# Optimization experiments

Measured on AMD Instinct MI355X. Metric: run time of the kernel, lower is better.

The kernel has to match this reference:

```python
import jax, jax.numpy as jnp
import numpy as np

B, N, K, NUM_CLASSES = 8, 4096, 20, 40


def _knn_idx(x, k):
    # x: [B, N, D] -> indices of k nearest neighbors (self excluded), [B, N, k]
    sq = jnp.sum(x * x, axis=-1)  # [B, N]
    dist = sq[:, :, None] + sq[:, None, :] - 2.0 * jnp.einsum('bnd,bmd->bnm', x, x)
    dist = jnp.where(jnp.eye(x.shape[1], dtype=bool)[None], jnp.inf, dist)
    return jax.lax.top_k(-dist, k)[1]


def _edge_conv(x, idx, params):
    # PyG EdgeConv with max aggregation: max_j MLP([x_i, x_j - x_i])
    x_j = jax.vmap(lambda xb, ib: xb[ib])(x, idx)              # [B, N, K, D]
    x_i = jnp.broadcast_to(x[:, :, None, :], x_j.shape)        # [B, N, K, D]
    h = jnp.concatenate([x_i, x_j - x_i], axis=-1)             # [B, N, K, 2D]
    for w, b in params:
        h = jax.nn.relu(h @ w + b)
    return jnp.max(h, axis=2)                                  # [B, N, out]


def setup_inputs() -> dict:
    key = jax.random.key(0)
    ks = jax.random.split(key, 12)

    def lin(k, i, o):  # torch Linear default init
        k1, k2 = jax.random.split(k)
        s = 1.0 / np.sqrt(i)
        return (jax.random.uniform(k1, (i, o), jnp.float32, -s, s),
                jax.random.uniform(k2, (o,), jnp.float32, -s, s))

    inp = {
        'pos': jax.random.normal(ks[0], (B * N, 3), jnp.float32),
        'batch': jnp.repeat(jnp.arange(B, dtype=jnp.int32), N),
    }
    names = [('m1w1', 'm1b1', 6, 64), ('m1w2', 'm1b2', 64, 64), ('m1w3', 'm1b3', 64, 64),
             ('m2w1', 'm2b1', 128, 128), ('m2w2', 'm2b2', 128, 128), ('m2w3', 'm2b3', 128, 256),
             ('lin0_w', 'lin0_b', 256, 512), ('lin1_w', 'lin1_b', 512, 256),
             ('lin2_w', 'lin2_b', 256, 256), ('lin3_w', 'lin3_b', 256, NUM_CLASSES)]
    for t, (wn, bn, i, o) in enumerate(names):
        w, b = lin(ks[t + 1], i, o)
        inp[wn] = w
        inp[bn] = b
    return inp


def reference(pos, batch, m1w1, m1b1, m1w2, m1b2, m1w3, m1b3,
              m2w1, m2b1, m2w2, m2b2, m2w3, m2b3,
              lin0_w, lin0_b, lin1_w, lin1_b, lin2_w, lin2_b, lin3_w, lin3_b):
    x = pos.reshape(B, N, 3)
    x = _edge_conv(x, _knn_idx(x, K), [(m1w1, m1b1), (m1w2, m1b2), (m1w3, m1b3)])   # [B,N,64]
    x = _edge_conv(x, _knn_idx(x, K), [(m2w1, m2b1), (m2w2, m2b2), (m2w3, m2b3)])   # [B,N,256]
    x = jax.nn.relu(x @ lin0_w + lin0_b)                                            # [B,N,512]
    x = jax.ops.segment_max(x.reshape(B * N, -1), batch, num_segments=B)            # [B,512]
    x = jax.nn.relu(x @ lin1_w + lin1_b)
    x = jax.nn.relu(x @ lin2_w + lin2_b)   # dropout is identity in eval mode
    x = x @ lin3_w + lin3_b
    return jax.nn.log_softmax(x, axis=-1)
```

## Files before the change

kernel.cpp:

```cpp
#include <hip/hip_runtime.h>

#define DEVI static __device__ __forceinline__

typedef __attribute__((ext_vector_type(4))) float f32x4;
typedef __attribute__((ext_vector_type(8))) short short8;
typedef __attribute__((ext_vector_type(4))) short short4v;
typedef __attribute__((ext_vector_type(4))) unsigned uint4v;
typedef __attribute__((ext_vector_type(8))) __bf16 bf16x8;

#define N_    4096
#define KNN_  20
#define NPTS  32768

DEVI unsigned short f2bf(float f){
  unsigned u = __float_as_uint(f);
  u += 0x7FFFu + ((u >> 16) & 1u);
  return (unsigned short)(u >> 16);
}
DEVI float bf2f(unsigned short s){ return __uint_as_float(((unsigned)s) << 16); }
DEVI float bf2fs(short s){ return __uint_as_float(((unsigned)(unsigned short)s) << 16); }
DEVI unsigned umin32(unsigned a, unsigned b){ return a < b ? a : b; }
DEVI unsigned umax32(unsigned a, unsigned b){ return a > b ? a : b; }

DEVI f32x4 mfma16(short8 a, short8 b, f32x4 c){
  return __builtin_amdgcn_mfma_f32_16x16x32_bf16(
      __builtin_bit_cast(bf16x8, a), __builtin_bit_cast(bf16x8, b), c, 0, 0, 0);
}

DEVI short8 lds_frag(const unsigned short* buf, int row, int k0, int strideS, int swzMask){
  return *(const short8*)(buf + row*strideS + (k0 ^ ((row & swzMask) << 3)));
}
DEVI void lds_put8(unsigned short* buf, int row, int k0, int strideS, int swzMask, short8 v){
  *(short8*)(buf + row*strideS + (k0 ^ ((row & swzMask) << 3))) = v;
}
DEVI void lds_put1(unsigned short* buf, int row, int col, int strideS, int swzMask, unsigned short v){
  buf[row*strideS + (col ^ ((row & swzMask) << 3))] = v;
}

DEVI void ins32(unsigned K, unsigned (&a)[20]){
#pragma unroll
  for (int t = 19; t >= 1; --t) a[t] = umin32(a[t], umax32(a[t-1], K));
  a[0] = umin32(a[0], K);
}
DEVI void ins64(double K, double (&a)[20]){
#pragma unroll
  for (int t = 19; t >= 1; --t) a[t] = fmin(a[t], fmax(a[t-1], K));
  a[0] = fmin(a[0], K);
}

__global__ __launch_bounds__(256) void p3_k(const float* __restrict__ pos,
    unsigned short* __restrict__ p3h, unsigned short* __restrict__ p3l, float* __restrict__ nrm3){
  int p = blockIdx.x*256 + threadIdx.x;
  if (p >= NPTS) return;
  float x = pos[(size_t)p*3], y = pos[(size_t)p*3+1], z = pos[(size_t)p*3+2];
  float v[8] = {x, y, z, 0.f, 0.f, 0.f, 0.f, 0.f};
#pragma unroll
  for (int c = 0; c < 8; ++c){
    unsigned short h = f2bf(v[c]);
    p3h[(size_t)p*8 + c] = h;
    p3l[(size_t)p*8 + c] = f2bf(v[c] - bf2f(h));
  }
  nrm3[p] = fmaf(x, x, fmaf(y, y, z*z));
}

template<int MODE>
__global__ __launch_bounds__(256) void knn_k(const unsigned short* __restrict__ Xh,
                                             const unsigned short* __restrict__ Xl,
                                             const float* __restrict__ nrm,
                                             unsigned* __restrict__ pk){
  constexpr int OBL  = MODE ? 8192  : 1024;
  constexpr int OS   = MODE ? 16384 : 2048;
  constexpr int OBUF = OS + 17408;
  constexpr int OTHR = OBUF + 6144;
  constexpr int OSQ  = OTHR + 256;
  __shared__ __align__(16) char smem[OSQ + 256];
  unsigned short* Bh = (unsigned short*)(smem);
  unsigned short* Bl = (unsigned short*)(smem + OBL);
  unsigned* S        = (unsigned*)(smem + OS);
  unsigned* buf      = (unsigned*)(smem + OBUF);
  unsigned* rowThr   = (unsigned*)(smem + OTHR);
  float* sqj         = (float*)(smem + OSQ);
  unsigned* mD       = (unsigned*)(smem);

  const int blk = blockIdx.x;
  const int rt = blk & 63, ch = (blk >> 6) & 1, bb = blk >> 7;
  const int rowbase = rt * 64, cbase = ch * 2048;
  const size_t gb = (size_t)bb * N_;
  const int tid = threadIdx.x, lane = tid & 63, wid = tid >> 6;
  const int l15 = lane & 15, kL = (lane >> 4) << 3, r0 = (lane >> 4) << 2;

  if (tid < 64) rowThr[tid] = 0xFFFFFFFFu;

  short8 ah0 = {0,0,0,0,0,0,0,0}, ah1 = {0,0,0,0,0,0,0,0};
  short8 al0 = {0,0,0,0,0,0,0,0}, al1 = {0,0,0,0,0,0,0,0};
  const int arow = rowbase + (wid << 4) + l15;
  if (MODE == 1){
    const size_t ab = (gb + arow) * 64;
    ah0 = *(const short8*)(Xh + ab + kL);
    ah1 = *(const short8*)(Xh + ab + 32 + kL);
    al0 = *(const short8*)(Xl + ab + kL);
    al1 = *(const short8*)(Xl + ab + 32 + kL);
  } else {
    if (lane < 16){
      const size_t ab = (gb + arow) * 8;
      ah0 = *(const short8*)(Xh + ab);
      al0 = *(const short8*)(Xl + ab);
    }
  }
  float sqi[4];
#pragma unroll
  for (int r = 0; r < 4; ++r) sqi[r] = nrm[gb + rowbase + (wid << 4) + r0 + r];

  unsigned arr[20];
#pragma unroll
  for (int t = 0; t < 20; ++t) arr[t] = 0xFFFFFFFFu;
  int cnt = 0;
  const int srow = tid & 63, q = tid >> 6;

  if (MODE == 1){
    for (int f = tid; f < 512; f += 256){
      int lf = f & 63, half = (f >> 6) & 1, nt = f >> 7;
      int row = nt*16 + (lf & 15);
      int col = half*32 + ((lf >> 4) << 3);
      const size_t src = (gb + cbase + row) * 64 + col;
      *(short8*)(Bh + f*8) = *(const short8*)(Xh + src);
      *(short8*)(Bl + f*8) = *(const short8*)(Xl + src);
    }
  } else {
    if (tid < 64)       *(short8*)(Bh + tid*8)      = *(const short8*)(Xh + (gb + cbase + tid)*8);
    else if (tid < 128) *(short8*)(Bl + (tid-64)*8) = *(const short8*)(Xl + (gb + cbase + (tid-64))*8);
  }
  if (tid < 64) sqj[tid] = nrm[gb + cbase + tid];
  __syncthreads();

  for (int c = 0; c < 32; ++c){
    const bool selfTile = (cbase + c*64 == rowbase);
#pragma unroll
    for (int nt = 0; nt < 4; ++nt){
      f32x4 acc = {0.f,0.f,0.f,0.f};
      if (MODE == 1){
        const int fb = lane*8;
        short8 bh0 = *(const short8*)(Bh + (nt*2+0)*512 + fb);
        short8 bh1 = *(const short8*)(Bh + (nt*2+1)*512 + fb);
        short8 bl0 = *(const short8*)(Bl + (nt*2+0)*512 + fb);
        short8 bl1 = *(const short8*)(Bl + (nt*2+1)*512 + fb);
        acc = mfma16(ah0, bh0, acc); acc = mfma16(ah1, bh1, acc);
        acc = mfma16(ah0, bl0, acc); acc = mfma16(ah1, bl1, acc);
        acc = mfma16(al0, bh0, acc); acc = mfma16(al1, bh1, acc);
      } else {
        int br = nt*16 + l15;
        short8 bh = {0,0,0,0,0,0,0,0}, bl = {0,0,0,0,0,0,0,0};
        if (lane < 16){
          bh = *(const short8*)(Bh + br*8);
          bl = *(const short8*)(Bl + br*8);
        }
        acc = mfma16(ah0, bh, acc);
        acc = mfma16(ah0, bl, acc);
        acc = mfma16(al0, bh, acc);
      }
      int col = nt*16 + l15;
      float sj = sqj[col];
      unsigned cid = (unsigned)(c*64 + col);
#pragma unroll
      for (int r = 0; r < 4; ++r){
        int row = (wid << 4) + r0 + r;
        float dv = fmaxf(fmaf(-2.f, acc[r], sqi[r] + sj), 0.f);
        unsigned kb = (__float_as_uint(dv) & ~0x7FFu) | cid;
        if (selfTile && col == row) kb = 0x7F800000u | cid;
        S[row*68 + col] = kb;
      }
    }
    short8 nh0 = {0,0,0,0,0,0,0,0}, nh1 = {0,0,0,0,0,0,0,0};
    short8 nl0 = {0,0,0,0,0,0,0,0}, nl1 = {0,0,0,0,0,0,0,0};
    float nsq = 0.f;
    const bool more = (c + 1 < 32);
    if (more){
      if (MODE == 1){
#pragma unroll
        for (int ff = 0; ff < 2; ++ff){
          int f = tid + ff*256;
          int lf = f & 63, half = (f >> 6) & 1, nt = f >> 7;
          int row = nt*16 + (lf & 15);
          int col = half*32 + ((lf >> 4) << 3);
          const size_t src = (gb + cbase + (c+1)*64 + row) * 64 + col;
          if (ff == 0){ nh0 = *(const short8*)(Xh + src); nl0 = *(const short8*)(Xl + src); }
          else        { nh1 = *(const short8*)(Xh + src); nl1 = *(const short8*)(Xl + src); }
        }
      } else {
        if (tid < 64)       nh0 = *(const short8*)(Xh + (gb + cbase + (c+1)*64 + tid)*8);
        else if (tid < 128) nl0 = *(const short8*)(Xl + (gb + cbase + (c+1)*64 + (tid-64))*8);
      }
      if (tid < 64) nsq = nrm[gb + cbase + (c+1)*64 + tid];
    }
    __syncthreads();
    if (more){
      if (MODE == 1){
        *(short8*)(Bh + tid*8)       = nh0;
        *(short8*)(Bh + (tid+256)*8) = nh1;
        *(short8*)(Bl + tid*8)       = nl0;
        *(short8*)(Bl + (tid+256)*8) = nl1;
      } else {
        if (tid < 64)       *(short8*)(Bh + tid*8)      = nh0;
        else if (tid < 128) *(short8*)(Bl + (tid-64)*8) = nl0;
      }
      if (tid < 64) sqj[tid] = nsq;
    }
    {
      unsigned thrP = rowThr[srow];
      const uint4v* Sr4 = (const uint4v*)(S + srow*68 + q*16);
#pragma unroll
      for (int u4 = 0; u4 < 4; ++u4){
        uint4v v = Sr4[u4];
#pragma unroll
        for (int e = 0; e < 4; ++e){
          unsigned kb = v[e];
          if (kb < thrP){
            if (cnt < 6){ buf[cnt*256 + tid] = kb; ++cnt; }
            else ins32(kb, arr);
          }
        }
      }
      for (int t = 0; t < cnt; ++t) ins32(buf[t*256 + tid], arr);
      cnt = 0;
      atomicMin(&rowThr[srow], arr[19]);
    }
    __syncthreads();
  }
  if (q > 0){
#pragma unroll
    for (int t = 0; t < 20; ++t) mD[(srow*3 + q-1)*20 + t] = arr[t];
  }
  __syncthreads();
  if (q == 0){
    for (int qq = 0; qq < 3; ++qq)
#pragma unroll
      for (int t = 0; t < 20; ++t) ins32(mD[(srow*3 + qq)*20 + t], arr);
    const size_t gp = gb + rowbase + srow;
#pragma unroll
    for (int t = 0; t < 20; ++t) pk[((size_t)(ch*20 + t))*NPTS + gp] = arr[t];
  }
}

__global__ __launch_bounds__(256) void knn_merge_k(const unsigned* __restrict__ pk,
                                                   int* __restrict__ idx){
  const int p = blockIdx.x*256 + threadIdx.x;
  double arr[20];
#pragma unroll
  for (int t = 0; t < 20; ++t){
    unsigned k = pk[(size_t)t*NPTS + p];
    unsigned long long K = (((unsigned long long)(k & ~0x7FFu)) << 1) | (k & 0x7FFu);
    arr[t] = __builtin_bit_cast(double, K);
  }
#pragma unroll
  for (int t = 0; t < 20; ++t){
    unsigned k = pk[(size_t)(20 + t)*NPTS + p];
    unsigned long long K = (((unsigned long long)(k & ~0x7FFu)) << 1) | (2048u + (k & 0x7FFu));
    ins64(__builtin_bit_cast(double, K), arr);
  }
  int* o = idx + (size_t)p*KNN_;
#pragma unroll
  for (int t = 0; t < 20; ++t)
    o[t] = (int)(__builtin_bit_cast(unsigned long long, arr[t]) & 0xFFFu);
}

__global__ void stage_w_k(const float* __restrict__ src, unsigned short* __restrict__ dh,
                          unsigned short* __restrict__ dl, int K, int Nw, int KT, int NT){
  int tid = blockIdx.x*256 + threadIdx.x;
  if (tid >= NT*KT*64) return;
  int l = tid & 63;
  int kk = (tid >> 6) % KT;
  int nt = tid / (64*KT);
  int n = nt*16 + (l & 15);
  int kb = kk*32 + ((l >> 4) << 3);
#pragma unroll
  for (int e=0;e<8;++e){
    int k = kb + e;
    float w = (k < K) ? src[(size_t)k*Nw + n] : 0.f;
    unsigned short h = f2bf(w);
    dh[(size_t)tid*8 + e] = h;
    if (dl) dl[(size_t)tid*8 + e] = f2bf(w - bf2f(h));
  }
}

__global__ __launch_bounds__(256) void ec1_k(const float* __restrict__ pos, const int* __restrict__ idx1,
    const unsigned short* __restrict__ W1h, const unsigned short* __restrict__ W1l,
    const unsigned short* __restrict__ W2h, const unsigned short* __restrict__ W2l,
    const unsigned short* __restrict__ W3h, const unsigned short* __restrict__ W3l,
    const float* __restrict__ b1, const float* __restrict__ b2, const float* __restrict__ b3,
    unsigned short* __restrict__ x1h, unsigned short* __restrict__ x1l, float* __restrict__ nrm1){
  __shared__ __align__(16) char smem[52224];
  unsigned short* Ah  = (unsigned short*)(smem);
  unsigned short* Al  = (unsigned short*)(smem + 5120);
  unsigned short* H1h = (unsigned short*)(smem + 10240);
  unsigned short* H1l = (unsigned short*)(smem + 20480);
  unsigned short* H2h = (unsigned short*)(smem + 30720);
  unsigned short* H2l = (unsigned short*)(smem + 40960);
  unsigned* pmax = (unsigned*)(smem + 51200);
  const int p0 = blockIdx.x * 4;
  const int bb = p0 >> 12;
  const int tid = threadIdx.x, lane = tid & 63, wid = tid >> 6;
  pmax[tid] = 0u;
  if (tid < 80){
    int p = p0 + tid/20, slot = tid%20;
    int j = idx1[(size_t)p*KNN_ + slot];
    int gj = (bb << 12) + j;
    float a6[6];
    a6[0] = pos[(size_t)p*3]; a6[1] = pos[(size_t)p*3+1]; a6[2] = pos[(size_t)p*3+2];
    a6[3] = pos[(size_t)gj*3]   - a6[0];
    a6[4] = pos[(size_t)gj*3+1] - a6[1];
    a6[5] = pos[(size_t)gj*3+2] - a6[2];
#pragma unroll
    for (int q=0;q<4;++q){
      short8 vh, vl;
#pragma unroll
      for (int c=0;c<8;++c){
        int cc = q*8+c;
        float v = 0.f;
        if (cc < 6) v = a6[cc];
        unsigned short h = f2bf(v);
        vh[c] = (short)h;
        vl[c] = (short)f2bf(v - bf2f(h));
      }
      lds_put8(Ah, tid, q*8, 32, 3, vh);
      lds_put8(Al, tid, q*8, 32, 3, vl);
    }
  }
  __syncthreads();
  const int l15 = lane & 15, kL = (lane >> 4) << 3, r0 = (lane >> 4) << 2;
  {
    int nt = wid;
    short8 wh = *(const short8*)(W1h + ((size_t)nt*64 + lane)*8);
    short8 wl = *(const short8*)(W1l + ((size_t)nt*64 + lane)*8);
    float bias = b1[nt*16 + l15];
    for (int mt=0; mt<5; ++mt){
      int ar = mt*16 + l15;
      short8 ah = lds_frag(Ah, ar, kL, 32, 3);
      short8 al = lds_frag(Al, ar, kL, 32, 3);
      f32x4 acc = {0.f,0.f,0.f,0.f};
      acc = mfma16(ah, wh, acc);
      acc = mfma16(ah, wl, acc);
      acc = mfma16(al, wh, acc);
#pragma unroll
      for (int r=0;r<4;++r){
        int row = mt*16 + r0 + r;
        float v = fmaxf(acc[r] + bias, 0.f);
        unsigned short h = f2bf(v);
        lds_put1(H1h, row, nt*16+l15, 64, 7, h);
        lds_put1(H1l, row, nt*16+l15, 64, 7, f2bf(v - bf2f(h)));
      }
    }
  }
  __syncthreads();
  {
    int nt = wid;
    short8 wh0 = *(const short8*)(W2h + ((size_t)(nt*2+0)*64 + lane)*8);
    short8 wh1 = *(const short8*)(W2h + ((size_t)(nt*2+1)*64 + lane)*8);
    short8 wl0 = *(const short8*)(W2l + ((size_t)(nt*2+0)*64 + lane)*8);
    short8 wl1 = *(const short8*)(W2l + ((size_t)(nt*2+1)*64 + lane)*8);
    float bias = b2[nt*16 + l15];
    for (int mt=0; mt<5; ++mt){
      int ar = mt*16 + l15;
      short8 ah0 = lds_frag(H1h, ar, kL,      64, 7);
      short8 ah1 = lds_frag(H1h, ar, 32 + kL, 64, 7);
      short8 al0 = lds_frag(H1l, ar, kL,      64, 7);
      short8 al1 = lds_frag(H1l, ar, 32 + kL, 64, 7);
      f32x4 acc = {0.f,0.f,0.f,0.f};
      acc = mfma16(ah0, wh0, acc); acc = mfma16(ah1, wh1, acc);
      acc = mfma16(ah0, wl0, acc); acc = mfma16(ah1, wl1, acc);
      acc = mfma16(al0, wh0, acc); acc = mfma16(al1, wh1, acc);
#pragma unroll
      for (int r=0;r<4;++r){
        int row = mt*16 + r0 + r;
        float v = fmaxf(acc[r] + bias, 0.f);
        unsigned short h = f2bf(v);
        lds_put1(H2h, row, nt*16+l15, 64, 7, h);
        lds_put1(H2l, row, nt*16+l15, 64, 7, f2bf(v - bf2f(h)));
      }
    }
  }
  __syncthreads();
  {
    int nt = wid;
    short8 wh0 = *(const short8*)(W3h + ((size_t)(nt*2+0)*64 + lane)*8);
    short8 wh1 = *(const short8*)(W3h + ((size_t)(nt*2+1)*64 + lane)*8);
    short8 wl0 = *(const short8*)(W3l + ((size_t)(nt*2+0)*64 + lane)*8);
    short8 wl1 = *(const short8*)(W3l + ((size_t)(nt*2+1)*64 + lane)*8);
    float bias = b3[nt*16 + l15];
    for (int mt=0; mt<5; ++mt){
      int ar = mt*16 + l15;
      short8 ah0 = lds_frag(H2h, ar, kL,      64, 7);
      short8 ah1 = lds_frag(H2h, ar, 32 + kL, 64, 7);
      short8 al0 = lds_frag(H2l, ar, kL,      64, 7);
      short8 al1 = lds_frag(H2l, ar, 32 + kL, 64, 7);
      f32x4 acc = {0.f,0.f,0.f,0.f};
      acc = mfma16(ah0, wh0, acc); acc = mfma16(ah1, wh1, acc);
      acc = mfma16(ah0, wl0, acc); acc = mfma16(ah1, wl1, acc);
      acc = mfma16(al0, wh0, acc); acc = mfma16(al1, wh1, acc);
#pragma unroll
      for (int r=0;r<4;++r){
        int row = mt*16 + r0 + r;
        float v = fmaxf(acc[r] + bias, 0.f);
        atomicMax(&pmax[(row/20)*64 + nt*16 + l15], __float_as_uint(v));
      }
    }
  }
  __syncthreads();
  if (tid < 128){
    int p = tid >> 5, cp = tid & 31;
    int c0 = cp*2, c1 = c0 + 1;
    float m0 = __uint_as_float(pmax[p*64 + c0]);
    float m1 = __uint_as_float(pmax[p*64 + c1]);
    int gp = p0 + p;
    unsigned short h0 = f2bf(m0), h1v = f2bf(m1);
    x1h[(size_t)gp*64 + c0] = h0;
    x1h[(size_t)gp*64 + c1] = h1v;
    x1l[(size_t)gp*64 + c0] = f2bf(m0 - bf2f(h0));
    x1l[(size_t)gp*64 + c1] = f2bf(m1 - bf2f(h1v));
    float s = fmaf(m0, m0, m1*m1);
    s += __shfl_xor(s, 1, 32); s += __shfl_xor(s, 2, 32); s += __shfl_xor(s, 4, 32);
    s += __shfl_xor(s, 8, 32); s += __shfl_xor(s, 16, 32);
    if (cp == 0) nrm1[gp] = s;
  }
}

__global__ __launch_bounds__(256) void ec2_k(const unsigned short* __restrict__ x1h, const int* __restrict__ idx2,
    const unsigned short* __restrict__ V1, const unsigned short* __restrict__ V2, const unsigned short* __restrict__ V3,
    const float* __restrict__ b1, const float* __restrict__ b2, const float* __restrict__ b3,
    unsigned short* __restrict__ x2b){
  __shared__ __align__(16) char smem[81920];
  unsigned short* A  = (unsigned short*)(smem);
  unsigned short* H1 = (unsigned short*)(smem + 40960);
  const int p0 = blockIdx.x * 8, bb = p0 >> 12;
  const int tid = threadIdx.x, lane = tid & 63, wid = tid >> 6;
  const int l15 = lane & 15, r0 = (lane >> 4) << 2;

  if (tid < 160){
    int p = p0 + tid/20, slot = tid%20;
    int j = idx2[(size_t)p*KNN_ + slot];
    int gj = (bb << 12) + j;
    const unsigned short* xi = x1h + (size_t)p*64;
    const unsigned short* xj = x1h + (size_t)gj*64;
    int mt = tid >> 4, lrow = tid & 15;
#pragma unroll
    for (int q=0;q<8;++q){
      short8 vi = *(const short8*)(xi + q*8);
      short8 vj = *(const short8*)(xj + q*8);
      short8 vd;
#pragma unroll
      for (int c=0;c<8;++c) vd[c] = (short)f2bf(bf2fs(vj[c]) - bf2fs(vi[c]));
      *(short8*)(A + (((mt*4 + (q>>2))*64) + (q&3)*16 + lrow)*8) = vi;
      *(short8*)(A + (((mt*4 + 2 + (q>>2))*64) + (q&3)*16 + lrow)*8) = vd;
    }
  }
  __syncthreads();

  {
    short8 w[2][4];
#pragma unroll
    for (int ni=0;ni<2;++ni)
#pragma unroll
      for (int kk=0;kk<4;++kk)
        w[ni][kk] = *(const short8*)(V1 + ((size_t)((wid*2+ni)*4+kk)*64 + lane)*8);
    f32x4 b4[2];
    b4[0] = *(const f32x4*)(b1 + (wid*2+0)*16 + r0);
    b4[1] = *(const f32x4*)(b1 + (wid*2+1)*16 + r0);
    for (int mt=0; mt<10; ++mt){
      short8 bfr[4];
#pragma unroll
      for (int kk=0;kk<4;++kk) bfr[kk] = *(const short8*)(A + ((mt*4+kk)*64 + lane)*8);
#pragma unroll
      for (int ni=0;ni<2;++ni){
        int nt = wid*2 + ni;
        f32x4 acc = {0.f,0.f,0.f,0.f};
#pragma unroll
        for (int kk=0;kk<4;++kk) acc = mfma16(w[ni][kk], bfr[kk], acc);
        short4v v4;
#pragma unroll
        for (int r=0;r<4;++r) v4[r] = (short)f2bf(fmaxf(acc[r] + b4[ni][r], 0.f));
        int kk2 = nt >> 1, sub2 = (nt & 1)*2 + (r0 >> 3);
        *(short4v*)(H1 + ((mt*4+kk2)*64 + sub2*16 + l15)*8 + (r0 & 4)) = v4;
      }
    }
  }
  __syncthreads();
  {
    short8 w[2][4];
#pragma unroll
    for (int ni=0;ni<2;++ni)
#pragma unroll
      for (int kk=0;kk<4;++kk)
        w[ni][kk] = *(const short8*)(V2 + ((size_t)((wid*2+ni)*4+kk)*64 + lane)*8);
    f32x4 b4[2];
    b4[0] = *(const f32x4*)(b2 + (wid*2+0)*16 + r0);
    b4[1] = *(const f32x4*)(b2 + (wid*2+1)*16 + r0);
    for (int mt=0; mt<10; ++mt){
      short8 bfr[4];
#pragma unroll
      for (int kk=0;kk<4;++kk) bfr[kk] = *(const short8*)(H1 + ((mt*4+kk)*64 + lane)*8);
#pragma unroll
      for (int ni=0;ni<2;++ni){
        int nt = wid*2 + ni;
        f32x4 acc = {0.f,0.f,0.f,0.f};
#pragma unroll
        for (int kk=0;kk<4;++kk) acc = mfma16(w[ni][kk], bfr[kk], acc);
        short4v v4;
#pragma unroll
        for (int r=0;r<4;++r) v4[r] = (short)f2bf(fmaxf(acc[r] + b4[ni][r], 0.f));
        int kk2 = nt >> 1, sub2 = (nt & 1)*2 + (r0 >> 3);
        *(short4v*)(A + ((mt*4+kk2)*64 + sub2*16 + l15)*8 + (r0 & 4)) = v4;
      }
    }
  }
  __syncthreads();
  for (int g2=0; g2<2; ++g2){
    {
      short8 w[2][4];
#pragma unroll
      for (int ni=0;ni<2;++ni)
#pragma unroll
        for (int kk=0;kk<4;++kk)
          w[ni][kk] = *(const short8*)(V3 + ((size_t)((g2*8 + wid*2+ni)*4+kk)*64 + lane)*8);
      f32x4 b4[2];
      b4[0] = *(const f32x4*)(b3 + (g2*8 + wid*2+0)*16 + r0);
      b4[1] = *(const f32x4*)(b3 + (g2*8 + wid*2+1)*16 + r0);
      for (int mt=0; mt<10; ++mt){
        short8 bfr[4];
#pragma unroll
        for (int kk=0;kk<4;++kk) bfr[kk] = *(const short8*)(A + ((mt*4+kk)*64 + lane)*8);
#pragma unroll
        for (int ni=0;ni<2;++ni){
          int ntl = wid*2 + ni;
          f32x4 acc = {0.f,0.f,0.f,0.f};
#pragma unroll
          for (int kk=0;kk<4;++kk) acc = mfma16(w[ni][kk], bfr[kk], acc);
          short4v v4;
#pragma unroll
          for (int r=0;r<4;++r) v4[r] = (short)f2bf(fmaxf(acc[r] + b4[ni][r], 0.f));
          int kk2 = ntl >> 1, sub2 = (ntl & 1)*2 + (r0 >> 3);
          *(short4v*)(H1 + ((mt*4+kk2)*64 + sub2*16 + l15)*8 + (r0 & 4)) = v4;
        }
      }
    }
    __syncthreads();
    if (tid < 128){
      int p = tid >> 4, c8 = tid & 15;
      int kk = c8 >> 2, sub = c8 & 3;
      unsigned short mx[8];
#pragma unroll
      for (int e=0;e<8;++e) mx[e] = 0;
      for (int e=0;e<20;++e){
        int ee = e + p + c8; ee -= (ee >= 20) ? 20 : 0; ee -= (ee >= 20) ? 20 : 0;
        int row = p*20 + ee;
        short8 v = *(const short8*)(H1 + (((row>>4)*4 + kk)*64 + sub*16 + (row & 15))*8);
#pragma unroll
        for (int k2=0;k2<8;++k2){
          unsigned short u = (unsigned short)v[k2];
          mx[k2] = u > mx[k2] ? u : mx[k2];
        }
      }
      short8 o;
#pragma unroll
      for (int k2=0;k2<8;++k2) o[k2] = (short)mx[k2];
      *(short8*)(x2b + (size_t)(p0 + p)*256 + g2*128 + c8*8) = o;
    }
    __syncthreads();
  }
}

__global__ __launch_bounds__(256) void lin0_k(const unsigned short* __restrict__ x2b, const unsigned short* __restrict__ W0s,
                                              const float* __restrict__ b0, unsigned* __restrict__ pool){
  __shared__ __align__(16) char smem[67584];
  unsigned short* A = (unsigned short*)(smem);
  unsigned* ploc = (unsigned*)(smem + 65536);
  const int blk = blockIdx.x; const size_t row0 = (size_t)blk * 128; const int bb = blk >> 5;
  const int tid = threadIdx.x, lane = tid & 63, wid = tid >> 6;
  for (int it = tid; it < 4096; it += 256){
    int row = it >> 5, q = (it & 31) << 3;
    lds_put8(A, row, q, 256, 7, *(const short8*)(x2b + (row0 + row)*256 + q));
  }
  ploc[tid] = 0u; ploc[tid+256] = 0u;
  __syncthreads();
  const int l15 = lane & 15, kL = (lane >> 4) << 3;
  short8 af[2][8];
#pragma unroll
  for (int m=0;m<2;++m)
#pragma unroll
    for (int kk=0;kk<8;++kk)
      af[m][kk] = lds_frag(A, (wid*2+m)*16 + l15, kk*32 + kL, 256, 7);
  for (int nt=0; nt<32; ++nt){
    f32x4 a0 = {0.f,0.f,0.f,0.f}, a1 = {0.f,0.f,0.f,0.f};
#pragma unroll
    for (int kk=0;kk<8;++kk){
      short8 w = *(const short8*)(W0s + ((size_t)(nt*8+kk)*64 + lane)*8);
      a0 = mfma16(af[0][kk], w, a0);
      a1 = mfma16(af[1][kk], w, a1);
    }
    int col = nt*16 + l15;
    float m = fmaxf(fmaxf(fmaxf(a0[0],a0[1]),fmaxf(a0[2],a0[3])),
                    fmaxf(fmaxf(a1[0],a1[1]),fmaxf(a1[2],a1[3])));
    m = fmaxf(m + b0[col], 0.f);
    atomicMax(&ploc[col], __float_as_uint(m));
  }
  __syncthreads();
  atomicMax(&pool[(size_t)bb*512 + tid], ploc[tid]);
  atomicMax(&pool[(size_t)bb*512 + tid + 256], ploc[tid+256]);
}

__global__ __launch_bounds__(256) void head_k(const unsigned* __restrict__ pool,
    const float* __restrict__ w1, const float* __restrict__ bb1,
    const float* __restrict__ w2, const float* __restrict__ bb2,
    const float* __restrict__ w3, const float* __restrict__ bb3,
    float* __restrict__ out){
  __shared__ float pl[8*512];
  __shared__ float y1[8*256];
  __shared__ float y2[8*256];
  __shared__ float lg[8*40];
  const int tid = threadIdx.x;
  for (int it = tid; it < 4096; it += 256) pl[it] = __uint_as_float(pool[it]);
  __syncthreads();
  {
    float acc[8]; float bv = bb1[tid];
#pragma unroll
    for (int r=0;r<8;++r) acc[r] = bv;
    for (int k=0;k<512;++k){
      float w = w1[(size_t)k*256 + tid];
#pragma unroll
      for (int r=0;r<8;++r) acc[r] = fmaf(pl[r*512+k], w, acc[r]);
    }
#pragma unroll
    for (int r=0;r<8;++r) y1[r*256+tid] = fmaxf(acc[r], 0.f);
  }
  __syncthreads();
  {
    float acc[8]; float bv = bb2[tid];
#pragma unroll
    for (int r=0;r<8;++r) acc[r] = bv;
    for (int k=0;k<256;++k){
      float w = w2[(size_t)k*256 + tid];
#pragma unroll
      for (int r=0;r<8;++r) acc[r] = fmaf(y1[r*256+k], w, acc[r]);
    }
#pragma unroll
    for (int r=0;r<8;++r) y2[r*256+tid] = fmaxf(acc[r], 0.f);
  }
  __syncthreads();
  if (tid < 40){
    float acc[8]; float bv = bb3[tid];
#pragma unroll
    for (int r=0;r<8;++r) acc[r] = bv;
    for (int k=0;k<256;++k){
      float w = w3[(size_t)k*40 + tid];
#pragma unroll
      for (int r=0;r<8;++r) acc[r] = fmaf(y2[r*256+k], w, acc[r]);
    }
#pragma unroll
    for (int r=0;r<8;++r) lg[r*40+tid] = acc[r];
  }
  __syncthreads();
  if (tid < 8){
    float m = -__builtin_inff();
    for (int c2=0;c2<40;++c2) m = fmaxf(m, lg[tid*40+c2]);
    float s = 0.f;
    for (int c2=0;c2<40;++c2) s += expf(lg[tid*40+c2] - m);
    float L = logf(s);
    for (int c2=0;c2<40;++c2) out[tid*40+c2] = lg[tid*40+c2] - m - L;
  }
}

extern "C" void kernel_launch(void* const* d_in, const int* in_sizes, int n_in,
                              void* d_out, int out_size, void* d_ws, size_t ws_size,
                              hipStream_t stream){
  (void)in_sizes; (void)n_in; (void)out_size; (void)ws_size;
  const float* pos  = (const float*)d_in[0];
  const float* m1w1 = (const float*)d_in[2];  const float* m1b1 = (const float*)d_in[3];
  const float* m1w2 = (const float*)d_in[4];  const float* m1b2 = (const float*)d_in[5];
  const float* m1w3 = (const float*)d_in[6];  const float* m1b3 = (const float*)d_in[7];
  const float* m2w1 = (const float*)d_in[8];  const float* m2b1 = (const float*)d_in[9];
  const float* m2w2 = (const float*)d_in[10]; const float* m2b2 = (const float*)d_in[11];
  const float* m2w3 = (const float*)d_in[12]; const float* m2b3 = (const float*)d_in[13];
  const float* l0w  = (const float*)d_in[14]; const float* l0b  = (const float*)d_in[15];
  const float* l1w  = (const float*)d_in[16]; const float* l1b  = (const float*)d_in[17];
  const float* l2w  = (const float*)d_in[18]; const float* l2b  = (const float*)d_in[19];
  const float* l3w  = (const float*)d_in[20]; const float* l3b  = (const float*)d_in[21];

  char* ws = (char*)d_ws;
  size_t o = 0;
  auto alloc = [&](size_t bytes){ size_t r = o; o += (bytes + 255) & ~(size_t)255; return r; };
  size_t o_idx1 = alloc((size_t)NPTS*20*4);
  size_t o_idx2 = alloc((size_t)NPTS*20*4);
  size_t o_x1h  = alloc((size_t)NPTS*64*2);
  size_t o_x1l  = alloc((size_t)NPTS*64*2);
  size_t o_nrm  = alloc((size_t)NPTS*4);
  size_t o_x2b  = alloc((size_t)NPTS*256*2);
  size_t o_pool = alloc(8*512*4);
  size_t o_p3h  = alloc((size_t)NPTS*8*2);
  size_t o_p3l  = alloc((size_t)NPTS*8*2);
  size_t o_nrm3 = alloc((size_t)NPTS*4);
  size_t o_pk   = alloc((size_t)2*20*NPTS*4);
  size_t o_W1h = alloc(4*1*64*8*2),  o_W1l = alloc(4*1*64*8*2);
  size_t o_W2h = alloc(4*2*64*8*2),  o_W2l = alloc(4*2*64*8*2);
  size_t o_W3h = alloc(4*2*64*8*2),  o_W3l = alloc(4*2*64*8*2);
  size_t o_V1  = alloc(8*4*64*8*2);
  size_t o_V2  = alloc(8*4*64*8*2);
  size_t o_V3  = alloc(16*4*64*8*2);
  size_t o_W0  = alloc(32*8*64*8*2);

  hipMemsetAsync(ws + o_pool, 0, 8*512*4, stream);

  stage_w_k<<<1,256,0,stream>>>(m1w1, (unsigned short*)(ws+o_W1h), (unsigned short*)(ws+o_W1l), 6, 64, 1, 4);
  stage_w_k<<<2,256,0,stream>>>(m1w2, (unsigned short*)(ws+o_W2h), (unsigned short*)(ws+o_W2l), 64, 64, 2, 4);
  stage_w_k<<<2,256,0,stream>>>(m1w3, (unsigned short*)(ws+o_W3h), (unsigned short*)(ws+o_W3l), 64, 64, 2, 4);
  stage_w_k<<<8,256,0,stream>>>(m2w1, (unsigned short*)(ws+o_V1), nullptr, 128, 128, 4, 8);
  stage_w_k<<<8,256,0,stream>>>(m2w2, (unsigned short*)(ws+o_V2), nullptr, 128, 128, 4, 8);
  stage_w_k<<<16,256,0,stream>>>(m2w3, (unsigned short*)(ws+o_V3), nullptr, 128, 256, 4, 16);
  stage_w_k<<<64,256,0,stream>>>(l0w,  (unsigned short*)(ws+o_W0), nullptr, 256, 512, 8, 32);

  p3_k<<<128,256,0,stream>>>(pos, (unsigned short*)(ws+o_p3h), (unsigned short*)(ws+o_p3l), (float*)(ws+o_nrm3));

  knn_k<0><<<1024,256,0,stream>>>((const unsigned short*)(ws+o_p3h), (const unsigned short*)(ws+o_p3l),
                                  (const float*)(ws+o_nrm3), (unsigned*)(ws+o_pk));
  knn_merge_k<<<128,256,0,stream>>>((const unsigned*)(ws+o_pk), (int*)(ws+o_idx1));

  ec1_k<<<8192,256,0,stream>>>(pos, (const int*)(ws+o_idx1),
      (const unsigned short*)(ws+o_W1h), (const unsigned short*)(ws+o_W1l),
      (const unsigned short*)(ws+o_W2h), (const unsigned short*)(ws+o_W2l),
      (const unsigned short*)(ws+o_W3h), (const unsigned short*)(ws+o_W3l),
      m1b1, m1b2, m1b3,
      (unsigned short*)(ws+o_x1h), (unsigned short*)(ws+o_x1l), (float*)(ws+o_nrm));

  knn_k<1><<<1024,256,0,stream>>>((const unsigned short*)(ws+o_x1h), (const unsigned short*)(ws+o_x1l),
                                  (const float*)(ws+o_nrm), (unsigned*)(ws+o_pk));
  knn_merge_k<<<128,256,0,stream>>>((const unsigned*)(ws+o_pk), (int*)(ws+o_idx2));

  ec2_k<<<4096,256,0,stream>>>((const unsigned short*)(ws+o_x1h), (const int*)(ws+o_idx2),
      (const unsigned short*)(ws+o_V1), (const unsigned short*)(ws+o_V2), (const unsigned short*)(ws+o_V3),
      m2b1, m2b2, m2b3, (unsigned short*)(ws+o_x2b));

  lin0_k<<<256,256,0,stream>>>((const unsigned short*)(ws+o_x2b), (const unsigned short*)(ws+o_W0),
                               l0b, (unsigned*)(ws+o_pool));

  head_k<<<1,256,0,stream>>>((const unsigned*)(ws+o_pool), l1w, l1b, l2w, l2b, l3w, l3b, (float*)d_out);
}
```

Baseline: 655.4 us.

## Transpose KNN MFMA so each lane holds its query's distances in registers

The kNN distance tile is computed transposed (candidates as the A operand, queries as B), so each lane's accumulator holds four candidate distances for one fixed query row. The lane filters its 16 distance keys straight from registers instead of writing them to a shared-memory score tile and reading them back. This drops the S staging buffer, its LDS traffic and shared-memory footprint, and moves the candidate selection before the barrier. The final merge now combines partial lists across the four lane groups of each query.

Result: no change. 656.1 us (+0.1%).

```diff
diff --git a/kernel.cpp b/kernel.cpp
--- a/kernel.cpp
+++ b/kernel.cpp
@@ -5,7 +5,6 @@
 typedef __attribute__((ext_vector_type(4))) float f32x4;
 typedef __attribute__((ext_vector_type(8))) short short8;
 typedef __attribute__((ext_vector_type(4))) short short4v;
-typedef __attribute__((ext_vector_type(4))) unsigned uint4v;
 typedef __attribute__((ext_vector_type(8))) __bf16 bf16x8;
 
 #define N_    4096
@@ -69,14 +68,13 @@
                                              const float* __restrict__ nrm,
                                              unsigned* __restrict__ pk){
   constexpr int OBL  = MODE ? 8192  : 1024;
-  constexpr int OS   = MODE ? 16384 : 2048;
-  constexpr int OBUF = OS + 17408;
+  constexpr int OBUF = MODE ? 16384 : 2048;
   constexpr int OTHR = OBUF + 6144;
   constexpr int OSQ  = OTHR + 256;
-  __shared__ __align__(16) char smem[OSQ + 256];
+  constexpr int SM   = MODE ? (OSQ + 256) : 15488;
+  __shared__ __align__(16) char smem[SM];
   unsigned short* Bh = (unsigned short*)(smem);
   unsigned short* Bl = (unsigned short*)(smem + OBL);
-  unsigned* S        = (unsigned*)(smem + OS);
   unsigned* buf      = (unsigned*)(smem + OBUF);
   unsigned* rowThr   = (unsigned*)(smem + OTHR);
   float* sqj         = (float*)(smem + OSQ);
@@ -87,40 +85,40 @@
   const int rowbase = rt * 64, cbase = ch * 2048;
   const size_t gb = (size_t)bb * N_;
   const int tid = threadIdx.x, lane = tid & 63, wid = tid >> 6;
-  const int l15 = lane & 15, kL = (lane >> 4) << 3, r0 = (lane >> 4) << 2;
+  const int l15 = lane & 15, g = lane >> 4, kL = g << 3, r0 = g << 2;
+  const int qidx = wid*16 + l15;
 
   if (tid < 64) rowThr[tid] = 0xFFFFFFFFu;
 
-  short8 ah0 = {0,0,0,0,0,0,0,0}, ah1 = {0,0,0,0,0,0,0,0};
-  short8 al0 = {0,0,0,0,0,0,0,0}, al1 = {0,0,0,0,0,0,0,0};
-  const int arow = rowbase + (wid << 4) + l15;
+  short8 qh0 = {0,0,0,0,0,0,0,0}, qh1 = {0,0,0,0,0,0,0,0};
+  short8 ql0 = {0,0,0,0,0,0,0,0}, ql1 = {0,0,0,0,0,0,0,0};
   if (MODE == 1){
-    const size_t ab = (gb + arow) * 64;
-    ah0 = *(const short8*)(Xh + ab + kL);
-    ah1 = *(const short8*)(Xh + ab + 32 + kL);
-    al0 = *(const short8*)(Xl + ab + kL);
-    al1 = *(const short8*)(Xl + ab + 32 + kL);
+    const size_t ab = (gb + rowbase + qidx) * 64;
+    qh0 = *(const short8*)(Xh + ab + kL);
+    qh1 = *(const short8*)(Xh + ab + 32 + kL);
+    ql0 = *(const short8*)(Xl + ab + kL);
+    ql1 = *(const short8*)(Xl + ab + 32 + kL);
   } else {
-    if (lane < 16){
-      const size_t ab = (gb + arow) * 8;
-      ah0 = *(const short8*)(Xh + ab);
-      al0 = *(const short8*)(Xl + ab);
-    }
-  }
-  float sqi[4];
-#pragma unroll
-  for (int r = 0; r < 4; ++r) sqi[r] = nrm[gb + rowbase + (wid << 4) + r0 + r];
+    if (g == 0){
+      const size_t ab = (gb + rowbase + qidx) * 8;
+      qh0 = *(const short8*)(Xh + ab);
+      ql0 = *(const short8*)(Xl + ab);
+    }
+  }
+  const float si = nrm[gb + rowbase + qidx];
 
   unsigned arr[20];
 #pragma unroll
   for (int t = 0; t < 20; ++t) arr[t] = 0xFFFFFFFFu;
   int cnt = 0;
-  const int srow = tid & 63, q = tid >> 6;
+  bool selfR[4];
+#pragma unroll
+  for (int r = 0; r < 4; ++r) selfR[r] = (l15 == r0 + r);
 
   if (MODE == 1){
     for (int f = tid; f < 512; f += 256){
-      int lf = f & 63, half = (f >> 6) & 1, nt = f >> 7;
-      int row = nt*16 + (lf & 15);
+      int lf = f & 63, half = (f >> 6) & 1, ct = f >> 7;
+      int row = ct*16 + (lf & 15);
       int col = half*32 + ((lf >> 4) << 3);
       const size_t src = (gb + cbase + row) * 64 + col;
       *(short8*)(Bh + f*8) = *(const short8*)(Xh + src);
@@ -135,39 +133,37 @@
 
   for (int c = 0; c < 32; ++c){
     const bool selfTile = (cbase + c*64 == rowbase);
-#pragma unroll
-    for (int nt = 0; nt < 4; ++nt){
+    unsigned kb16[16];
+#pragma unroll
+    for (int ct = 0; ct < 4; ++ct){
       f32x4 acc = {0.f,0.f,0.f,0.f};
       if (MODE == 1){
         const int fb = lane*8;
-        short8 bh0 = *(const short8*)(Bh + (nt*2+0)*512 + fb);
-        short8 bh1 = *(const short8*)(Bh + (nt*2+1)*512 + fb);
-        short8 bl0 = *(const short8*)(Bl + (nt*2+0)*512 + fb);
-        short8 bl1 = *(const short8*)(Bl + (nt*2+1)*512 + fb);
-        acc = mfma16(ah0, bh0, acc); acc = mfma16(ah1, bh1, acc);
-        acc = mfma16(ah0, bl0, acc); acc = mfma16(ah1, bl1, acc);
-        acc = mfma16(al0, bh0, acc); acc = mfma16(al1, bh1, acc);
+        short8 ch0 = *(const short8*)(Bh + (ct*2+0)*512 + fb);
+        short8 ch1 = *(const short8*)(Bh + (ct*2+1)*512 + fb);
+        short8 cl0 = *(const short8*)(Bl + (ct*2+0)*512 + fb);
+        short8 cl1 = *(const short8*)(Bl + (ct*2+1)*512 + fb);
+        acc = mfma16(ch0, qh0, acc); acc = mfma16(ch1, qh1, acc);
+        acc = mfma16(cl0, qh0, acc); acc = mfma16(cl1, qh1, acc);
+        acc = mfma16(ch0, ql0, acc); acc = mfma16(ch1, ql1, acc);
       } else {
-        int br = nt*16 + l15;
-        short8 bh = {0,0,0,0,0,0,0,0}, bl = {0,0,0,0,0,0,0,0};
-        if (lane < 16){
-          bh = *(const short8*)(Bh + br*8);
-          bl = *(const short8*)(Bl + br*8);
+        short8 cb = {0,0,0,0,0,0,0,0}, cl_ = {0,0,0,0,0,0,0,0};
+        if (g == 0){
+          cb  = *(const short8*)(Bh + (ct*16 + l15)*8);
+          cl_ = *(const short8*)(Bl + (ct*16 + l15)*8);
         }
-        acc = mfma16(ah0, bh, acc);
-        acc = mfma16(ah0, bl, acc);
-        acc = mfma16(al0, bh, acc);
-      }
-      int col = nt*16 + l15;
-      float sj = sqj[col];
-      unsigned cid = (unsigned)(c*64 + col);
+        acc = mfma16(cb,  qh0, acc);
+        acc = mfma16(cl_, qh0, acc);
+        acc = mfma16(cb,  ql0, acc);
+      }
+      f32x4 sj4 = *(const f32x4*)(sqj + ct*16 + r0);
 #pragma unroll
       for (int r = 0; r < 4; ++r){
-        int row = (wid << 4) + r0 + r;
-        float dv = fmaxf(fmaf(-2.f, acc[r], sqi[r] + sj), 0.f);
+        unsigned cid = (unsigned)(c*64 + ct*16 + r0 + r);
+        float dv = fmaxf(fmaf(-2.f, acc[r], si + sj4[r]), 0.f);
         unsigned kb = (__float_as_uint(dv) & ~0x7FFu) | cid;
-        if (selfTile && col == row) kb = 0x7F800000u | cid;
-        S[row*68 + col] = kb;
+        if (selfTile && ct == wid && selfR[r]) kb = 0x7F800000u | cid;
+        kb16[ct*4 + r] = kb;
       }
     }
     short8 nh0 = {0,0,0,0,0,0,0,0}, nh1 = {0,0,0,0,0,0,0,0};
@@ -179,8 +175,8 @@
 #pragma unroll
         for (int ff = 0; ff < 2; ++ff){
           int f = tid + ff*256;
-          int lf = f & 63, half = (f >> 6) & 1, nt = f >> 7;
-          int row = nt*16 + (lf & 15);
+          int lf = f & 63, half = (f >> 6) & 1, ct = f >> 7;
+          int row = ct*16 + (lf & 15);
           int col = half*32 + ((lf >> 4) << 3);
           const size_t src = (gb + cbase + (c+1)*64 + row) * 64 + col;
           if (ff == 0){ nh0 = *(const short8*)(Xh + src); nl0 = *(const short8*)(Xl + src); }
@@ -191,6 +187,20 @@
         else if (tid < 128) nl0 = *(const short8*)(Xl + (gb + cbase + (c+1)*64 + (tid-64))*8);
       }
       if (tid < 64) nsq = nrm[gb + cbase + (c+1)*64 + tid];
+    }
+    {
+      unsigned thrP = rowThr[qidx];
+#pragma unroll
+      for (int i = 0; i < 16; ++i){
+        unsigned kb = kb16[i];
+        if (kb < thrP){
+          if (cnt < 6){ buf[cnt*256 + tid] = kb; ++cnt; }
+          else ins32(kb, arr);
+        }
+      }
+      for (int t = 0; t < cnt; ++t) ins32(buf[t*256 + tid], arr);
+      cnt = 0;
+      atomicMin(&rowThr[qidx], arr[19]);
     }
     __syncthreads();
     if (more){
@@ -205,37 +215,19 @@
       }
       if (tid < 64) sqj[tid] = nsq;
     }
-    {
-      unsigned thrP = rowThr[srow];
-      const uint4v* Sr4 = (const uint4v*)(S + srow*68 + q*16);
-#pragma unroll
-      for (int u4 = 0; u4 < 4; ++u4){
-        uint4v v = Sr4[u4];
-#pragma unroll
-        for (int e = 0; e < 4; ++e){
-          unsigned kb = v[e];
-          if (kb < thrP){
-            if (cnt < 6){ buf[cnt*256 + tid] = kb; ++cnt; }
-            else ins32(kb, arr);
-          }
-        }
-      }
-      for (int t = 0; t < cnt; ++t) ins32(buf[t*256 + tid], arr);
-      cnt = 0;
-      atomicMin(&rowThr[srow], arr[19]);
-    }
     __syncthreads();
   }
-  if (q > 0){
-#pragma unroll
-    for (int t = 0; t < 20; ++t) mD[(srow*3 + q-1)*20 + t] = arr[t];
-  }
-  __syncthreads();
-  if (q == 0){
-    for (int qq = 0; qq < 3; ++qq)
-#pragma unroll
-      for (int t = 0; t < 20; ++t) ins32(mD[(srow*3 + qq)*20 + t], arr);
-    const size_t gp = gb + rowbase + srow;
+  __syncthreads();
+  if (g > 0){
+#pragma unroll
+    for (int t = 0; t < 20; ++t) mD[(qidx*3 + g-1)*20 + t] = arr[t];
+  }
+  __syncthreads();
+  if (g == 0){
+    for (int gg = 0; gg < 3; ++gg)
+#pragma unroll
+      for (int t = 0; t < 20; ++t) ins32(mD[(qidx*3 + gg)*20 + t], arr);
+    const size_t gp = gb + rowbase + qidx;
 #pragma unroll
     for (int t = 0; t < 20; ++t) pk[((size_t)(ch*20 + t))*NPTS + gp] = arr[t];
   }
```
